# Performance work log

Measured on AMD Instinct MI355X. Metric: run time of the kernel, lower is better.

Reference implementation:

```python
import jax, jax.numpy as jnp
import numpy as np

WIN = 7
SHIFT = 3
HEADS = 6
EPS = 1e-5


def _rel_pos_index(ws):
    coords = np.stack(np.meshgrid(np.arange(ws), np.arange(ws), indexing='ij')).reshape(2, -1)
    rel = (coords[:, :, None] - coords[:, None, :]).transpose(1, 2, 0)  # (N, N, 2)
    rel[..., 0] += ws - 1
    rel[..., 1] += ws - 1
    rel[..., 0] *= 2 * ws - 1
    return jnp.asarray(rel.sum(-1).reshape(-1))  # (N*N,)


def _attn_mask(H, W, ws, ss):
    img = np.zeros((H, W))
    sl = (slice(0, -ws), slice(-ws, -ss), slice(-ss, None))
    cnt = 0
    for hs in sl:
        for wss in sl:
            img[hs, wss] = cnt
            cnt += 1
    mw = img.reshape(H // ws, ws, W // ws, ws).transpose(0, 2, 1, 3).reshape(-1, ws * ws)
    am = mw[:, None, :] - mw[:, :, None]  # (nw, N, N): mw[j]-mw[i]
    return jnp.asarray(np.where(am != 0, -1e9, 0.0).astype(np.float32))


def _layernorm(x, g, b):
    mu = x.mean(-1, keepdims=True)
    var = ((x - mu) ** 2).mean(-1, keepdims=True)
    return (x - mu) * jax.lax.rsqrt(var + EPS) * g + b


def setup_inputs() -> dict:
    key = jax.random.key(0)
    ks = jax.random.split(key, 6)
    B, H, W, C = 4, 224, 224, 192
    return {
        'x': jax.random.normal(ks[0], (B, H * W, C), jnp.float32),
        'norm1_g': jnp.ones((C,), jnp.float32),
        'norm1_b': jnp.zeros((C,), jnp.float32),
        'qkv_w': jax.random.normal(ks[1], (C, 3 * C), jnp.float32) * 0.02,
        'qkv_b': jnp.zeros((3 * C,), jnp.float32),
        'rpb_table': jax.random.normal(ks[2], ((2 * WIN - 1) ** 2, HEADS), jnp.float32) * 0.02,
        'proj_w': jax.random.normal(ks[3], (C, C), jnp.float32) * 0.02,
        'proj_b': jnp.zeros((C,), jnp.float32),
        'norm2_g': jnp.ones((C,), jnp.float32),
        'norm2_b': jnp.zeros((C,), jnp.float32),
        'fc1_w': jax.random.normal(ks[4], (C, 4 * C), jnp.float32) * 0.02,
        'fc1_b': jnp.zeros((4 * C,), jnp.float32),
        'fc2_w': jax.random.normal(ks[5], (4 * C, C), jnp.float32) * 0.02,
        'fc2_b': jnp.zeros((C,), jnp.float32),
        'h': 224,
        'w': 224,
    }


def reference(x, norm1_g, norm1_b, qkv_w, qkv_b, rpb_table, proj_w, proj_b,
              norm2_g, norm2_b, fc1_w, fc1_b, fc2_w, fc2_b, h, w):
    B, L, C = x.shape
    ch = C // HEADS
    N = WIN * WIN
    nh, nw = h // WIN, w // WIN
    rel_idx = _rel_pos_index(WIN)
    mask = _attn_mask(h, w, WIN, SHIFT)  # (nh*nw, N, N)

    shortcut = x
    xn = _layernorm(x, norm1_g, norm1_b).reshape(B, h, w, C)
    xs = jnp.roll(xn, (-SHIFT, -SHIFT), axis=(1, 2))
    # window partition -> (B*nh*nw, N, C)
    xw = xs.reshape(B, nh, WIN, nw, WIN, C).transpose(0, 1, 3, 2, 4, 5).reshape(B * nh * nw, N, C)

    qkv = (xw @ qkv_w + qkv_b).reshape(-1, N, 3, HEADS, ch).transpose(2, 0, 3, 1, 4)
    q, k, v = qkv[0], qkv[1], qkv[2]  # (NW, HEADS, N, ch)
    scale = ch ** -0.5
    attn = jnp.einsum('whic,whjc->whij', q * scale, k)
    bias = rpb_table[rel_idx].reshape(N, N, HEADS).transpose(2, 0, 1)  # (HEADS, N, N)
    attn = attn + bias[None]
    attn = attn.reshape(B, nh * nw, HEADS, N, N) + mask[None, :, None]
    attn = jax.nn.softmax(attn, axis=-1).reshape(B * nh * nw, HEADS, N, N)

    out = jnp.einsum('whij,whjc->whic', attn, v).transpose(0, 2, 1, 3).reshape(-1, N, C)
    out = out @ proj_w + proj_b
    # window reverse + roll back
    out = out.reshape(B, nh, nw, WIN, WIN, C).transpose(0, 1, 3, 2, 4, 5).reshape(B, h, w, C)
    out = jnp.roll(out, (SHIFT, SHIFT), axis=(1, 2)).reshape(B, L, C)

    x = shortcut + out
    xn2 = _layernorm(x, norm2_g, norm2_b)
    hid = jax.nn.gelu(xn2 @ fc1_w + fc1_b, approximate=False)
    return x + (hid @ fc2_w + fc2_b)
```

## Files before the change

kernel.cpp:

```cpp
#include <hip/hip_runtime.h>
#include <stdint.h>

#define MB    50176
#define CDIM  192

typedef __attribute__((ext_vector_type(8))) short bf16x8;
typedef __attribute__((ext_vector_type(4))) float f32x4;

#define WFENCE asm volatile("s_waitcnt lgkmcnt(0)" ::: "memory")

__device__ __forceinline__ float wsum(float v){
  #pragma unroll
  for (int m=32;m>=1;m>>=1) v += __shfl_xor(v,m,64);
  return v;
}
__device__ __forceinline__ float bfbits2f(uint32_t h){
  union{uint32_t u; float f;} x; x.u = h<<16; return x.f;
}
__device__ __forceinline__ uint16_t f2bfbits(float f){
  union{float ff; uint32_t u;} x; x.ff = f;
  return (uint16_t)((x.u + 0x7FFFu + ((x.u>>16)&1u)) >> 16);
}
__device__ __forceinline__ void gload16(const void* g, void* l){
  __builtin_amdgcn_global_load_lds(
      (const __attribute__((address_space(1))) uint32_t*)g,
      (__attribute__((address_space(3))) uint32_t*)l, 16, 0, 0);
}
__device__ __forceinline__ size_t row2tok(int r_g){
  int widx = r_g/49, tpos = r_g - widx*49;
  int b = widx>>10, rem = widx&1023;
  int h = (rem>>5)*7 + tpos/7 + 3; if (h>=224) h-=224;
  int w = (rem&31)*7 + (tpos - (tpos/7)*7) + 3; if (w>=224) w-=224;
  return (size_t)b*MB + (size_t)h*224 + w;
}

__global__ __launch_bounds__(256) void prep_kernel(
    const float* __restrict__ qkv_w, const float* __restrict__ proj_w,
    const float* __restrict__ fc1_w, const float* __restrict__ fc2_w,
    const float* __restrict__ rpb,
    uint16_t* __restrict__ qkvW, uint16_t* __restrict__ prjW,
    uint16_t* __restrict__ fc1W, uint16_t* __restrict__ fc2W,
    float* __restrict__ btbl){
  int idx = blockIdx.x*256 + threadIdx.x;
  if (idx < 110592){ int k=idx/576, n=idx-k*576; qkvW[n*192+k]=f2bfbits(qkv_w[idx]); return; }
  idx -= 110592;
  if (idx < 36864){ int k=idx/192, n=idx-k*192; prjW[n*192+k]=f2bfbits(proj_w[idx]); return; }
  idx -= 36864;
  if (idx < 147456){ int k=idx/768, n=idx-k*768; fc1W[n*192+k]=f2bfbits(fc1_w[idx]); return; }
  idx -= 147456;
  if (idx < 147456){ int k=idx/192, n=idx-k*192; fc2W[n*768+k]=f2bfbits(fc2_w[idx]); return; }
  idx -= 147456;
  if (idx >= 98304) return;
  int j = idx & 63, i = (idx>>6) & 63;
  int hd = (idx>>12) % 6, cls = (idx>>12)/6;
  float v = -1e9f;
  if (i < 49 && j < 49){
    int dh = i/7 - j/7, dw = i%7 - j%7;
    v = rpb[((dh+6)*13 + (dw+6))*6 + hd];
    int cH = cls>>1, cW = cls&1;
    int li = (cH ? (i/7 < 4 ? 1 : 2) : 0)*3 + (cW ? (i%7 < 4 ? 1 : 2) : 0);
    int lj = (cH ? (j/7 < 4 ? 1 : 2) : 0)*3 + (cW ? (j%7 < 4 ? 1 : 2) : 0);
    if (li != lj) v = -1e9f;
  }
  btbl[idx] = v;
}

__global__ __launch_bounds__(256) void ln1_kernel(
    const float* __restrict__ x, const float* __restrict__ g,
    const float* __restrict__ bt, uint16_t* __restrict__ dst, int row0){
  int wid_l = (int)((blockIdx.x*256u + threadIdx.x) >> 6);
  int lane  = threadIdx.x & 63;
  size_t sidx = row2tok(row0 + wid_l);
  const float* s = x + sidx*CDIM;
  float v0=s[lane], v1=s[lane+64], v2=s[lane+128];
  float mu  = wsum(v0+v1+v2) * (1.f/192.f);
  float var = wsum(v0*v0+v1*v1+v2*v2)*(1.f/192.f) - mu*mu;
  float rs  = rsqrtf(var + 1e-5f);
  uint16_t* d = dst + (size_t)wid_l*CDIM;
  d[lane]     = f2bfbits((v0-mu)*rs*g[lane]     + bt[lane]);
  d[lane+64]  = f2bfbits((v1-mu)*rs*g[lane+64]  + bt[lane+64]);
  d[lane+128] = f2bfbits((v2-mu)*rs*g[lane+128] + bt[lane+128]);
}

enum { EPI_QKV=0, EPI_FC1=2, EPI_FC2=3 };

template<int EPI, int K, int NN>
__global__ __launch_bounds__(384) void mgemm(
    const uint16_t* __restrict__ A, const uint16_t* __restrict__ WT,
    const float* __restrict__ bias, void* __restrict__ outp,
    const float* __restrict__ resid, int row0){
  __shared__ __attribute__((aligned(16))) char As[128*128];
  __shared__ __attribute__((aligned(16))) char Bs[192*128];
  const int tid  = threadIdx.x;
  const int lane = tid & 63;
  const int wid  = tid >> 6;
  const int pm = wid / 3, pn = wid - pm*3;
  const int brow = blockIdx.y * 128;
  const int cbase = blockIdx.x * 192;
  const int srow = lane >> 3;
  const int sg   = (lane & 7) ^ srow;
  const int r16 = lane & 15, t4 = lane >> 4;

  f32x4 acc[4][4];
  #pragma unroll
  for (int m=0;m<4;m++)
    #pragma unroll
    for (int n=0;n<4;n++) acc[m][n] = (f32x4){0.f,0.f,0.f,0.f};

  for (int k0 = 0; k0 < K; k0 += 64){
    for (int ch = wid; ch < 40; ch += 6){
      if (ch < 16)
        gload16(A + (size_t)(brow + ch*8 + srow)*K + k0 + sg*8, As + ch*1024);
      else {
        int bc = ch - 16;
        gload16(WT + (size_t)(cbase + bc*8 + srow)*K + k0 + sg*8, Bs + bc*1024);
      }
    }
    __syncthreads();

    bf16x8 af[4][2], bfr[4][2];
    #pragma unroll
    for (int m=0;m<4;m++)
      #pragma unroll
      for (int ks=0;ks<2;ks++){
        int arow = pm*64 + m*16 + r16;
        af[m][ks] = *(const bf16x8*)(As + arow*128 + (((ks*4+t4) ^ (arow&7))<<4));
      }
    #pragma unroll
    for (int n=0;n<4;n++)
      #pragma unroll
      for (int ks=0;ks<2;ks++){
        int brn = pn*64 + n*16 + r16;
        bfr[n][ks] = *(const bf16x8*)(Bs + brn*128 + (((ks*4+t4) ^ (brn&7))<<4));
      }
    #pragma unroll
    for (int m=0;m<4;m++)
      #pragma unroll
      for (int n=0;n<4;n++)
        #pragma unroll
        for (int ks=0;ks<2;ks++)
          acc[m][n] = __builtin_amdgcn_mfma_f32_16x16x32_bf16(
              af[m][ks], bfr[n][ks], acc[m][n], 0, 0, 0);
    __syncthreads();
  }

  float bi[4];
  #pragma unroll
  for (int n=0;n<4;n++) bi[n] = bias[cbase + pn*64 + n*16 + r16];
  #pragma unroll
  for (int m=0;m<4;m++){
    #pragma unroll
    for (int j=0;j<4;j++){
      int r = brow + pm*64 + m*16 + t4*4 + j;
      if constexpr (EPI==EPI_QKV || EPI==EPI_FC1){
        #pragma unroll
        for (int n=0;n<4;n++){
          float v = acc[m][n][j] + bi[n];
          if constexpr (EPI==EPI_FC1)
            v = 0.5f*v*(1.f + erff(v*0.70710678118654752f));
          ((uint16_t*)outp)[(size_t)r*NN + cbase + pn*64 + n*16 + r16] = f2bfbits(v);
        }
      } else {
        size_t pr = row2tok(row0 + r)*CDIM;
        #pragma unroll
        for (int n=0;n<4;n++){
          size_t p = pr + cbase + pn*64 + n*16 + r16;
          ((float*)outp)[p] = acc[m][n][j] + bi[n] + resid[p];
        }
      }
    }
  }
}

__global__ __launch_bounds__(384) void proj_ln2(
    const uint16_t* __restrict__ A, const uint16_t* __restrict__ WT,
    const float* __restrict__ pbias, const float* __restrict__ x,
    const float* __restrict__ g2, const float* __restrict__ b2,
    float* __restrict__ xout, uint16_t* __restrict__ ln2out, int row0){
  __shared__ __attribute__((aligned(16))) char As[128*128];
  __shared__ __attribute__((aligned(16))) char Bs[192*128];
  __shared__ float stats[3][128][2];
  const int tid  = threadIdx.x;
  const int lane = tid & 63;
  const int wid  = tid >> 6;
  const int pm = wid / 3, pn = wid - pm*3;
  const int brow = blockIdx.x * 128;
  const int srow = lane >> 3;
  const int sg   = (lane & 7) ^ srow;
  const int lrow16 = lane & 15, lkh = lane >> 4;

  f32x4 acc[4][4];
  #pragma unroll
  for (int m=0;m<4;m++)
    #pragma unroll
    for (int n=0;n<4;n++) acc[m][n] = (f32x4){0.f,0.f,0.f,0.f};

  for (int k0 = 0; k0 < 192; k0 += 64){
    for (int ch = wid; ch < 16; ch += 6)
      gload16(A + (size_t)(brow + ch*8 + srow)*192 + k0 + sg*8, As + ch*1024);
    for (int ch = wid; ch < 24; ch += 6)
      gload16(WT + (size_t)(ch*8 + srow)*192 + k0 + sg*8, Bs + ch*1024);
    __syncthreads();

    bf16x8 af[4][2], bfr[4][2];
    #pragma unroll
    for (int m=0;m<4;m++)
      #pragma unroll
      for (int ks=0;ks<2;ks++){
        int arow = pm*64 + m*16 + lrow16;
        af[m][ks] = *(const bf16x8*)(As + arow*128 + (((ks*4+lkh) ^ (arow&7))<<4));
      }
    #pragma unroll
    for (int n=0;n<4;n++)
      #pragma unroll
      for (int ks=0;ks<2;ks++){
        int brn = pn*64 + n*16 + lrow16;
        bfr[n][ks] = *(const bf16x8*)(Bs + brn*128 + (((ks*4+lkh) ^ (brn&7))<<4));
      }
    #pragma unroll
    for (int m=0;m<4;m++)
      #pragma unroll
      for (int n=0;n<4;n++)
        #pragma unroll
        for (int ks=0;ks<2;ks++)
          acc[m][n] = __builtin_amdgcn_mfma_f32_16x16x32_bf16(
              af[m][ks], bfr[n][ks], acc[m][n], 0, 0, 0);
    __syncthreads();
  }

  float bi[4], g2v[4], b2v[4];
  #pragma unroll
  for (int n=0;n<4;n++){
    int c = pn*64 + n*16 + lrow16;
    bi[n] = pbias[c]; g2v[n] = g2[c]; b2v[n] = b2[c];
  }
  #pragma unroll
  for (int m=0;m<4;m++){
    #pragma unroll
    for (int j=0;j<4;j++){
      int r = pm*64 + m*16 + lkh*4 + j;
      size_t pr = row2tok(row0 + brow + r)*CDIM;
      float s1 = 0.f, s2 = 0.f;
      #pragma unroll
      for (int n=0;n<4;n++){
        int c = pn*64 + n*16 + lrow16;
        float y = acc[m][n][j] + bi[n] + x[pr + c];
        acc[m][n][j] = y;
        xout[pr + c] = y;
        s1 += y; s2 = fmaf(y, y, s2);
      }
      #pragma unroll
      for (int mk=1; mk<16; mk<<=1){
        s1 += __shfl_xor(s1, mk, 64);
        s2 += __shfl_xor(s2, mk, 64);
      }
      if (lrow16 == 0){ stats[pn][r][0] = s1; stats[pn][r][1] = s2; }
    }
  }
  __syncthreads();
  #pragma unroll
  for (int m=0;m<4;m++){
    #pragma unroll
    for (int j=0;j<4;j++){
      int r = pm*64 + m*16 + lkh*4 + j;
      float s1 = stats[0][r][0] + stats[1][r][0] + stats[2][r][0];
      float s2 = stats[0][r][1] + stats[1][r][1] + stats[2][r][1];
      float mu = s1*(1.f/192.f);
      float rs = rsqrtf(s2*(1.f/192.f) - mu*mu + 1e-5f);
      size_t pr = (size_t)(brow + r)*CDIM;
      #pragma unroll
      for (int n=0;n<4;n++){
        int c = pn*64 + n*16 + lrow16;
        ln2out[pr + c] = f2bfbits((acc[m][n][j]-mu)*rs*g2v[n] + b2v[n]);
      }
    }
  }
}

__global__ __launch_bounds__(256) void attn_kernel(
    const uint16_t* __restrict__ qkv, const float* __restrict__ btbl,
    uint16_t* __restrict__ attnout, int win0){
  const int wv   = threadIdx.x >> 6;
  const int lane = threadIdx.x & 63;
  const int whd  = blockIdx.x*4 + wv;
  const int widx = whd/6, hd = whd - widx*6;
  const int r16 = lane & 15, t4 = lane >> 4;
  __shared__ uint16_t Vt[4][32][72];
  __shared__ uint16_t Pl[4][16][72];

  #pragma unroll
  for (int e=lane; e<32*16; e+=64){ Vt[wv][e>>4][48 + (e&15)] = 0; }
  for (int ch = lane; ch < 196; ch += 64){
    int j = ch >> 2, c0 = (ch&3)*8;
    const uint16_t* src = qkv + ((size_t)widx*49 + j)*576 + hd*32 + 384 + c0;
    uint4 v = *(const uint4*)src;
    uint32_t u[4] = {v.x, v.y, v.z, v.w};
    #pragma unroll
    for (int q=0;q<8;q++) Vt[wv][c0+q][j] = (uint16_t)(u[q>>1] >> ((q&1)*16));
  }

  bf16x8 kf[4];
  #pragma unroll
  for (int jt=0;jt<4;jt++)
    kf[jt] = *(const bf16x8*)(qkv + ((size_t)widx*49 + jt*16 + r16)*576 + hd*32 + 192 + t4*8);

  const int gw = win0 + widx;
  const int cls = ((((gw&1023)>>5)==31)<<1) | ((gw&31)==31);
  const float* tb = btbl + ((size_t)(cls*6 + hd) << 12);
  const float scale = 0.17677669529663689f;

  WFENCE;
  bf16x8 bv[2][2];
  #pragma unroll
  for (int ct=0;ct<2;ct++)
    #pragma unroll
    for (int ks=0;ks<2;ks++)
      bv[ct][ks] = *(const bf16x8*)&Vt[wv][ct*16 + r16][ks*32 + t4*8];

  #pragma unroll 1
  for (int it=0; it<4; it++){
    bf16x8 qf = *(const bf16x8*)(qkv + ((size_t)widx*49 + it*16 + r16)*576 + hd*32 + t4*8);
    f32x4 acc[4];
    #pragma unroll
    for (int jt=0;jt<4;jt++){
      acc[jt] = (f32x4){0.f,0.f,0.f,0.f};
      acc[jt] = __builtin_amdgcn_mfma_f32_16x16x32_bf16(kf[jt], qf, acc[jt], 0,0,0);
    }
    int i = it*16 + r16;
    float s[4][4];
    float m = -3.4e38f;
    #pragma unroll
    for (int jt=0;jt<4;jt++){
      float4 bvv = *(const float4*)(tb + i*64 + jt*16 + t4*4);
      float bb[4] = {bvv.x, bvv.y, bvv.z, bvv.w};
      #pragma unroll
      for (int r=0;r<4;r++){
        s[jt][r] = acc[jt][r]*scale + bb[r];
        m = fmaxf(m, s[jt][r]);
      }
    }
    m = fmaxf(m, __shfl_xor(m, 16, 64));
    m = fmaxf(m, __shfl_xor(m, 32, 64));
    float sum = 0.f;
    #pragma unroll
    for (int jt=0;jt<4;jt++)
      #pragma unroll
      for (int r=0;r<4;r++){
        s[jt][r] = __expf(s[jt][r] - m);
        sum += s[jt][r];
      }
    sum += __shfl_xor(sum, 16, 64);
    sum += __shfl_xor(sum, 32, 64);
    float inv = 1.f / sum;
    #pragma unroll
    for (int jt=0;jt<4;jt++){
      uint32_t lo = (uint32_t)f2bfbits(s[jt][0]*inv) | ((uint32_t)f2bfbits(s[jt][1]*inv) << 16);
      uint32_t hi = (uint32_t)f2bfbits(s[jt][2]*inv) | ((uint32_t)f2bfbits(s[jt][3]*inv) << 16);
      *(uint2*)&Pl[wv][r16][jt*16 + t4*4] = make_uint2(lo, hi);
    }
    WFENCE;

    f32x4 o[2];
    o[0] = (f32x4){0.f,0.f,0.f,0.f};
    o[1] = (f32x4){0.f,0.f,0.f,0.f};
    #pragma unroll
    for (int ks=0;ks<2;ks++){
      bf16x8 pa = *(const bf16x8*)&Pl[wv][r16][ks*32 + t4*8];
      #pragma unroll
      for (int ct=0;ct<2;ct++)
        o[ct] = __builtin_amdgcn_mfma_f32_16x16x32_bf16(pa, bv[ct][ks], o[ct], 0,0,0);
    }
    #pragma unroll
    for (int r=0;r<4;r++){
      int i2 = it*16 + t4*4 + r;
      if (i2 < 49){
        size_t base = ((size_t)widx*49 + i2)*CDIM + hd*32;
        attnout[base + r16]      = f2bfbits(o[0][r]);
        attnout[base + 16 + r16] = f2bfbits(o[1][r]);
      }
    }
  }
}

extern "C" void kernel_launch(void* const* d_in, const int* in_sizes, int n_in,
                              void* d_out, int out_size, void* d_ws, size_t ws_size,
                              hipStream_t stream) {
  const float* x       = (const float*)d_in[0];
  const float* n1g     = (const float*)d_in[1];
  const float* n1b     = (const float*)d_in[2];
  const float* qkv_w   = (const float*)d_in[3];
  const float* qkv_b   = (const float*)d_in[4];
  const float* rpb     = (const float*)d_in[5];
  const float* proj_w  = (const float*)d_in[6];
  const float* proj_b  = (const float*)d_in[7];
  const float* n2g     = (const float*)d_in[8];
  const float* n2b     = (const float*)d_in[9];
  const float* fc1_w   = (const float*)d_in[10];
  const float* fc1_b   = (const float*)d_in[11];
  const float* fc2_w   = (const float*)d_in[12];
  const float* fc2_b   = (const float*)d_in[13];
  float* out = (float*)d_out;

  const size_t TBL = 221184 + 73728 + 294912 + 294912 + 393216;
  size_t need_full = (size_t)200704*CDIM*2 + (size_t)200704*768*2 + TBL;
  bool full = ws_size >= need_full;
  int T  = full ? 200704 : MB;
  int NC = full ? 1 : 4;
  int NW = T / 49;

  char* ws = (char*)d_ws;
  uint16_t* Abuf = (uint16_t*)ws;
  uint16_t* Bq   = (uint16_t*)(ws + (size_t)T*CDIM*2);
  char* wbase    = ws + (size_t)T*CDIM*2 + (size_t)T*768*2;
  uint16_t* qkvW = (uint16_t*)wbase;
  uint16_t* prjW = (uint16_t*)(wbase + 221184);
  uint16_t* fc1W = (uint16_t*)(wbase + 221184 + 73728);
  uint16_t* fc2W = (uint16_t*)(wbase + 221184 + 73728 + 294912);
  float*    btbl = (float*)(wbase + 221184 + 73728 + 294912 + 294912);

  prep_kernel<<<2112, 256, 0, stream>>>(qkv_w, proj_w, fc1_w, fc2_w, rpb,
                                        qkvW, prjW, fc1W, fc2W, btbl);

  for (int c = 0; c < NC; c++){
    int row0 = c*T, win0 = row0/49;
    ln1_kernel<<<T/4, 256, 0, stream>>>(x, n1g, n1b, Abuf, row0);
    mgemm<EPI_QKV, 192, 576>
        <<<dim3(3, T/128), 384, 0, stream>>>(Abuf, qkvW, qkv_b, (void*)Bq, nullptr, 0);
    attn_kernel<<<NW*6/4, 256, 0, stream>>>(Bq, btbl, Abuf, win0);
    proj_ln2<<<T/128, 384, 0, stream>>>(Abuf, prjW, proj_b, x, n2g, n2b,
                                        out, Abuf, row0);
    mgemm<EPI_FC1, 192, 768>
        <<<dim3(4, T/128), 384, 0, stream>>>(Abuf, fc1W, fc1_b, (void*)Bq, nullptr, 0);
    mgemm<EPI_FC2, 768, 192>
        <<<dim3(1, T/128), 384, 0, stream>>>(Bq, fc2W, fc2_b, (void*)out, out, row0);
  }
}
```

Measured before the change: 852.4 us.

## Retile GEMMs to 256x64 blocks with four waves and add sched barrier to fence

The generic GEMM kernel moves from 128x192 tiles with six waves to 256x64 tiles with four waves, each wave owning 64 rows and all 64 columns. The grid gains more column blocks, and the loads are restructured as fixed unrolled chunks per wave. A sched_barrier is also added to the WFENCE macro so the compiler cannot move instructions across the LDS wait. The retiling changes LDS reuse, since A is now reloaded for every 64-column slice. That raises A traffic and may shift occupancy or balance, and whether it helps depends on the row count T not shown here.

```diff
diff --git a/kernel.cpp b/kernel.cpp
--- a/kernel.cpp
+++ b/kernel.cpp
@@ -7,7 +7,8 @@
 typedef __attribute__((ext_vector_type(8))) short bf16x8;
 typedef __attribute__((ext_vector_type(4))) float f32x4;
 
-#define WFENCE asm volatile("s_waitcnt lgkmcnt(0)" ::: "memory")
+#define WFENCE do{ asm volatile("s_waitcnt lgkmcnt(0)" ::: "memory"); \
+                   __builtin_amdgcn_sched_barrier(0); }while(0)
 
 __device__ __forceinline__ float wsum(float v){
   #pragma unroll
@@ -85,18 +86,17 @@
 enum { EPI_QKV=0, EPI_FC1=2, EPI_FC2=3 };
 
 template<int EPI, int K, int NN>
-__global__ __launch_bounds__(384) void mgemm(
+__global__ __launch_bounds__(256) void mgemm(
     const uint16_t* __restrict__ A, const uint16_t* __restrict__ WT,
     const float* __restrict__ bias, void* __restrict__ outp,
     const float* __restrict__ resid, int row0){
-  __shared__ __attribute__((aligned(16))) char As[128*128];
-  __shared__ __attribute__((aligned(16))) char Bs[192*128];
+  __shared__ __attribute__((aligned(16))) char As[256*128];
+  __shared__ __attribute__((aligned(16))) char Bs[64*128];
   const int tid  = threadIdx.x;
   const int lane = tid & 63;
   const int wid  = tid >> 6;
-  const int pm = wid / 3, pn = wid - pm*3;
-  const int brow = blockIdx.y * 128;
-  const int cbase = blockIdx.x * 192;
+  const int brow = blockIdx.y * 256;
+  const int bcol = blockIdx.x * 64;
   const int srow = lane >> 3;
   const int sg   = (lane & 7) ^ srow;
   const int r16 = lane & 15, t4 = lane >> 4;
@@ -108,13 +108,15 @@
     for (int n=0;n<4;n++) acc[m][n] = (f32x4){0.f,0.f,0.f,0.f};
 
   for (int k0 = 0; k0 < K; k0 += 64){
-    for (int ch = wid; ch < 40; ch += 6){
-      if (ch < 16)
-        gload16(A + (size_t)(brow + ch*8 + srow)*K + k0 + sg*8, As + ch*1024);
-      else {
-        int bc = ch - 16;
-        gload16(WT + (size_t)(cbase + bc*8 + srow)*K + k0 + sg*8, Bs + bc*1024);
-      }
+    #pragma unroll
+    for (int c = 0; c < 8; c++){
+      int ch = wid*8 + c;
+      gload16(A + (size_t)(brow + ch*8 + srow)*K + k0 + sg*8, As + ch*1024);
+    }
+    #pragma unroll
+    for (int c = 0; c < 2; c++){
+      int ch = wid*2 + c;
+      gload16(WT + (size_t)(bcol + ch*8 + srow)*K + k0 + sg*8, Bs + ch*1024);
     }
     __syncthreads();
 
@@ -123,14 +125,14 @@
     for (int m=0;m<4;m++)
       #pragma unroll
       for (int ks=0;ks<2;ks++){
-        int arow = pm*64 + m*16 + r16;
+        int arow = wid*64 + m*16 + r16;
         af[m][ks] = *(const bf16x8*)(As + arow*128 + (((ks*4+t4) ^ (arow&7))<<4));
       }
     #pragma unroll
     for (int n=0;n<4;n++)
       #pragma unroll
       for (int ks=0;ks<2;ks++){
-        int brn = pn*64 + n*16 + r16;
+        int brn = n*16 + r16;
         bfr[n][ks] = *(const bf16x8*)(Bs + brn*128 + (((ks*4+t4) ^ (brn&7))<<4));
       }
     #pragma unroll
@@ -146,25 +148,25 @@
 
   float bi[4];
   #pragma unroll
-  for (int n=0;n<4;n++) bi[n] = bias[cbase + pn*64 + n*16 + r16];
+  for (int n=0;n<4;n++) bi[n] = bias[bcol + n*16 + r16];
   #pragma unroll
   for (int m=0;m<4;m++){
     #pragma unroll
     for (int j=0;j<4;j++){
-      int r = brow + pm*64 + m*16 + t4*4 + j;
+      int r = brow + wid*64 + m*16 + t4*4 + j;
       if constexpr (EPI==EPI_QKV || EPI==EPI_FC1){
         #pragma unroll
         for (int n=0;n<4;n++){
           float v = acc[m][n][j] + bi[n];
           if constexpr (EPI==EPI_FC1)
             v = 0.5f*v*(1.f + erff(v*0.70710678118654752f));
-          ((uint16_t*)outp)[(size_t)r*NN + cbase + pn*64 + n*16 + r16] = f2bfbits(v);
+          ((uint16_t*)outp)[(size_t)r*NN + bcol + n*16 + r16] = f2bfbits(v);
         }
       } else {
         size_t pr = row2tok(row0 + r)*CDIM;
         #pragma unroll
         for (int n=0;n<4;n++){
-          size_t p = pr + cbase + pn*64 + n*16 + r16;
+          size_t p = pr + bcol + n*16 + r16;
           ((float*)outp)[p] = acc[m][n][j] + bi[n] + resid[p];
         }
       }
@@ -425,13 +427,13 @@
     int row0 = c*T, win0 = row0/49;
     ln1_kernel<<<T/4, 256, 0, stream>>>(x, n1g, n1b, Abuf, row0);
     mgemm<EPI_QKV, 192, 576>
-        <<<dim3(3, T/128), 384, 0, stream>>>(Abuf, qkvW, qkv_b, (void*)Bq, nullptr, 0);
+        <<<dim3(9, T/256), 256, 0, stream>>>(Abuf, qkvW, qkv_b, (void*)Bq, nullptr, 0);
     attn_kernel<<<NW*6/4, 256, 0, stream>>>(Bq, btbl, Abuf, win0);
     proj_ln2<<<T/128, 384, 0, stream>>>(Abuf, prjW, proj_b, x, n2g, n2b,
                                         out, Abuf, row0);
     mgemm<EPI_FC1, 192, 768>
-        <<<dim3(4, T/128), 384, 0, stream>>>(Abuf, fc1W, fc1_b, (void*)Bq, nullptr, 0);
+        <<<dim3(12, T/256), 256, 0, stream>>>(Abuf, fc1W, fc1_b, (void*)Bq, nullptr, 0);
     mgemm<EPI_FC2, 768, 192>
-        <<<dim3(1, T/128), 384, 0, stream>>>(Bq, fc2W, fc2_b, (void*)out, out, row0);
-  }
-}
+        <<<dim3(3, T/256), 256, 0, stream>>>(Bq, fc2W, fc2_b, (void*)out, out, row0);
+  }
+}
```

Result: no change. 860.2 us (+0.9%).
